# Kernel optimization log

Hardware: AMD Instinct MI355X
Metric: run time of the kernel (lower is better)

## Reference

```python
import jax, jax.numpy as jnp
import numpy as np

DIM = 16
FDIM = 16
KNN = 10
N = 1_000_000


def setup_inputs() -> dict:
    key = jax.random.key(0)
    k1, k2, k3, k4, k5, k6 = jax.random.split(key, 6)
    xknn = jax.random.normal(k1, (N, DIM, KNN), dtype=jnp.float32)
    x = jax.random.normal(k2, (N, DIM), dtype=jnp.float32)
    # mlpF = Conv1d(dim, F, 1): weight [F, dim] (kernel size 1 squeezed), bias [F]
    s = 1.0 / np.sqrt(DIM)
    Wf = jax.random.normal(k3, (FDIM, DIM), dtype=jnp.float32) * s
    bf = jax.random.normal(k4, (FDIM,), dtype=jnp.float32) * s
    # mlp1 = Conv1d(F, 1, 1): weight [F], bias scalar
    s1 = 1.0 / np.sqrt(FDIM)
    W1 = jax.random.normal(k5, (FDIM,), dtype=jnp.float32) * s1
    b1 = jax.random.normal(k6, (), dtype=jnp.float32) * s1
    return {"xknn": xknn, "x": x, "Wf": Wf, "bf": bf, "W1": W1, "b1": b1}


def reference(xknn, x, Wf, bf, W1, b1):
    n = xknn.shape[0]
    x2 = xknn.reshape(n, DIM, KNN)                       # [N, dim, K]
    # mlpF on neighbors: Conv1d(dim->F, k=1)
    h2 = jnp.einsum('fd,ndk->nfk', Wf, x2) + bf[:, None]  # [N, F, K]
    a2 = jnp.einsum('f,nfk->nk', W1, h2)[:, None, :] + b1  # mlp1 -> [N, 1, K]
    # mlpF + mlp1 on center point
    x1 = x.reshape(n, DIM, 1)
    h1 = jnp.einsum('fd,ndk->nfk', Wf, x1) + bf[:, None]   # [N, F, 1]
    a1 = jnp.einsum('f,nfk->nk', W1, h1) + b1              # [N, 1] (squeeze+unsqueeze)
    # per-slice additive attention logits (the python loop in the original)
    logits = a2 + a1[:, :, None]                           # [N, 1, K]
    # torch Fn.softmax with implicit dim on 3D tensor -> dim=0 (faithful)
    xc = jax.nn.softmax(logits, axis=0)                    # [N, 1, K]
    # values: mlpF(x2) again, then a raw reshape [N,F,K]->[N,K,F] (not transpose)
    x2v = h2.reshape(n, KNN, FDIM)                         # [N, K, F]
    x_attn = jnp.matmul(xc, x2v)                           # [N, 1, F]
    return x_attn.squeeze(), x2v
```

## Files before the change

### kernel.cpp

```cpp
#include <hip/hip_runtime.h>
#include <math.h>


__device__ __forceinline__ void comb(float& m, float& s, float om, float os) {
  float M = fmaxf(m, om);
  if (M == -INFINITY) return;
  s = s * __expf(m - M) + os * __expf(om - M);
  m = M;
}

__global__ __launch_bounds__(256) void gap_k1(
    const float* __restrict__ xknn, const float* __restrict__ x,
    const float* __restrict__ Wf, const float* __restrict__ bf,
    const float* __restrict__ W1, const float* __restrict__ b1p,
    float* __restrict__ out, float* __restrict__ partials, int n) {
  __shared__ float s_x2[16][196];
  __shared__ float s_x[16][16];
  __shared__ float s_wf[256];
  __shared__ float s_misc[33];
  __shared__ float s_red[4][10][2];

  const int tid = threadIdx.x;
  const int p = tid >> 4;
  const int f = tid & 15;

  s_wf[tid] = Wf[tid];
  if (tid < 16) s_misc[tid] = bf[tid];
  else if (tid < 32) s_misc[tid] = W1[tid - 16];
  else if (tid == 32) s_misc[32] = b1p[0];
  __syncthreads();

  float wfrow[16];
#pragma unroll
  for (int d = 0; d < 16; ++d) wfrow[d] = s_wf[f * 16 + d];
  const float bff = s_misc[f];
  const float w1f = s_misc[16 + f];
  const float b1v = s_misc[32];

  float run_m = -INFINITY, run_s = 0.f;

  float* out0 = out;
  float* out1 = out + (size_t)n * 16;

  for (int base = blockIdx.x * 16; base < n; base += gridDim.x * 16) {
    __syncthreads();
    const int npts = min(16, n - base);
    const int nf4 = npts * 40;
    for (int idx4 = tid; idx4 < nf4; idx4 += 256) {
      float4 v = *(const float4*)(xknn + (size_t)base * 160 + (size_t)idx4 * 4);
      int pl = idx4 / 40;
      int r0 = (idx4 - pl * 40) * 4;
      float vv[4] = {v.x, v.y, v.z, v.w};
#pragma unroll
      for (int j = 0; j < 4; ++j) {
        int r = r0 + j;
        int d = r / 10;
        int kk = r - d * 10;
        s_x2[pl][d * 12 + kk] = vv[j];
      }
    }
    if (tid < npts * 4) {
      int pl = tid >> 2, c = tid & 3;
      *(float4*)(&s_x[pl][c * 4]) =
          *(const float4*)(x + (size_t)(base + pl) * 16 + (size_t)c * 4);
    }
    __syncthreads();

    float h2f[10];
#pragma unroll
    for (int k = 0; k < 10; ++k) h2f[k] = bff;
#pragma unroll
    for (int d = 0; d < 16; ++d) {
      const float* r = &s_x2[p][d * 12];
      float w = wfrow[d];
      float4 xa = *(const float4*)(r);
      float4 xb = *(const float4*)(r + 4);
      float2 xc2 = *(const float2*)(r + 8);
      h2f[0] = fmaf(w, xa.x, h2f[0]);
      h2f[1] = fmaf(w, xa.y, h2f[1]);
      h2f[2] = fmaf(w, xa.z, h2f[2]);
      h2f[3] = fmaf(w, xa.w, h2f[3]);
      h2f[4] = fmaf(w, xb.x, h2f[4]);
      h2f[5] = fmaf(w, xb.y, h2f[5]);
      h2f[6] = fmaf(w, xb.z, h2f[6]);
      h2f[7] = fmaf(w, xb.w, h2f[7]);
      h2f[8] = fmaf(w, xc2.x, h2f[8]);
      h2f[9] = fmaf(w, xc2.y, h2f[9]);
    }

    float a2[10];
#pragma unroll
    for (int k = 0; k < 10; ++k) a2[k] = w1f * h2f[k];
#pragma unroll
    for (int mask = 1; mask < 16; mask <<= 1) {
#pragma unroll
      for (int k = 0; k < 10; ++k) a2[k] += __shfl_xor(a2[k], mask, 16);
    }

    float h1f = bff;
#pragma unroll
    for (int d = 0; d < 16; ++d) h1f = fmaf(wfrow[d], s_x[p][d], h1f);
    float a1p = w1f * h1f;
#pragma unroll
    for (int mask = 1; mask < 16; mask <<= 1) a1p += __shfl_xor(a1p, mask, 16);

    const float addc = a1p + 2.0f * b1v;

    const int pt = base + p;
    if (pt < n) {
      float* o1 = out1 + (size_t)pt * 160 + f * 10;
      *(float2*)(o1 + 0) = make_float2(h2f[0], h2f[1]);
      *(float2*)(o1 + 2) = make_float2(h2f[2], h2f[3]);
      *(float2*)(o1 + 4) = make_float2(h2f[4], h2f[5]);
      *(float2*)(o1 + 6) = make_float2(h2f[6], h2f[7]);
      *(float2*)(o1 + 8) = make_float2(h2f[8], h2f[9]);
      if (f < 10) {
        float lsel = a2[0];
#pragma unroll
        for (int k = 1; k < 10; ++k) lsel = (f == k) ? a2[k] : lsel;
        lsel += addc;
        out0[(size_t)pt * 16 + f] = lsel;
        comb(run_m, run_s, lsel, 1.0f);
      }
    }
  }

#pragma unroll
  for (int mask = 16; mask < 64; mask <<= 1) {
    float om = __shfl_xor(run_m, mask, 64);
    float os = __shfl_xor(run_s, mask, 64);
    comb(run_m, run_s, om, os);
  }
  const int wave = tid >> 6, lane = tid & 63;
  __syncthreads();
  if (lane < 10) { s_red[wave][lane][0] = run_m; s_red[wave][lane][1] = run_s; }
  __syncthreads();
  if (tid < 10) {
    float m = s_red[0][tid][0], s = s_red[0][tid][1];
    comb(m, s, s_red[1][tid][0], s_red[1][tid][1]);
    comb(m, s, s_red[2][tid][0], s_red[2][tid][1]);
    comb(m, s, s_red[3][tid][0], s_red[3][tid][1]);
    partials[(size_t)blockIdx.x * 20 + tid * 2 + 0] = m;
    partials[(size_t)blockIdx.x * 20 + tid * 2 + 1] = s;
  }
}

__global__ __launch_bounds__(256) void gap_k2(const float* __restrict__ part,
                                              int nb, float* __restrict__ fin) {
  const int k = blockIdx.x;
  const int tid = threadIdx.x;
  float m = -INFINITY, s = 0.f;
  for (int i = tid; i < nb; i += 256)
    comb(m, s, part[(size_t)i * 20 + k * 2], part[(size_t)i * 20 + k * 2 + 1]);
#pragma unroll
  for (int mask = 1; mask < 64; mask <<= 1) {
    float om = __shfl_xor(m, mask, 64);
    float os = __shfl_xor(s, mask, 64);
    comb(m, s, om, os);
  }
  __shared__ float sm[4][2];
  const int wave = tid >> 6, lane = tid & 63;
  if (lane == 0) { sm[wave][0] = m; sm[wave][1] = s; }
  __syncthreads();
  if (tid == 0) {
    for (int w = 1; w < 4; ++w) comb(m, s, sm[w][0], sm[w][1]);
    fin[k * 2 + 0] = m;
    fin[k * 2 + 1] = s;
  }
}

__global__ __launch_bounds__(256) void gap_k3(const float* __restrict__ fin,
                                              float* __restrict__ out, int n) {
  __shared__ float s_fin[20];
  if (threadIdx.x < 20) s_fin[threadIdx.x] = fin[threadIdx.x];
  __syncthreads();
  float mk[10], rsk[10];
#pragma unroll
  for (int k = 0; k < 10; ++k) {
    mk[k] = s_fin[2 * k];
    rsk[k] = 1.0f / s_fin[2 * k + 1];
  }
  float* out0 = out;
  const float* out1 = out + (size_t)n * 16;
  const int q = threadIdx.x & 3;
  const int pl = threadIdx.x >> 2;
  for (long i = (long)blockIdx.x * 64 + pl; i < n; i += (long)gridDim.x * 64) {
    float* lrow = out0 + i * 16;
    float4 la = *(const float4*)(lrow);
    float4 lb = *(const float4*)(lrow + 4);
    float2 lc = *(const float2*)(lrow + 8);
    float l[10] = {la.x, la.y, la.z, la.w, lb.x, lb.y, lb.z, lb.w, lc.x, lc.y};
    float w[10];
#pragma unroll
    for (int k = 0; k < 10; ++k) w[k] = __expf(l[k] - mk[k]) * rsk[k];
    const float* vrow = out1 + i * 160 + q * 4;
    float4 acc = make_float4(0.f, 0.f, 0.f, 0.f);
#pragma unroll
    for (int k = 0; k < 10; ++k) {
      float4 v = *(const float4*)(vrow + k * 16);
      float wk = w[k];
      acc.x = fmaf(wk, v.x, acc.x);
      acc.y = fmaf(wk, v.y, acc.y);
      acc.z = fmaf(wk, v.z, acc.z);
      acc.w = fmaf(wk, v.w, acc.w);
    }
    *(float4*)(lrow + q * 4) = acc;
  }
}

extern "C" void kernel_launch(void* const* d_in, const int* in_sizes, int n_in,
                              void* d_out, int out_size, void* d_ws, size_t ws_size,
                              hipStream_t stream) {
  const float* xknn = (const float*)d_in[0];
  const float* x    = (const float*)d_in[1];
  const float* Wf   = (const float*)d_in[2];
  const float* bf   = (const float*)d_in[3];
  const float* W1   = (const float*)d_in[4];
  const float* b1   = (const float*)d_in[5];
  float* out = (float*)d_out;
  const int n = in_sizes[1] / 16;

  const int G1 = 2048;
  float* partials = (float*)d_ws;
  float* finals = partials + (size_t)G1 * 20;

  gap_k1<<<G1, 256, 0, stream>>>(xknn, x, Wf, bf, W1, b1, out, partials, n);
  gap_k2<<<10, 256, 0, stream>>>(partials, G1, finals);
  gap_k3<<<2048, 256, 0, stream>>>(finals, out, n);
}
```

Baseline: 584.5 us.

## Compute per-point features in registers with quad threads, dropping shared-memory staging

```diff
diff --git a/kernel.cpp b/kernel.cpp
--- a/kernel.cpp
+++ b/kernel.cpp
@@ -14,126 +14,140 @@
     const float* __restrict__ Wf, const float* __restrict__ bf,
     const float* __restrict__ W1, const float* __restrict__ b1p,
     float* __restrict__ out, float* __restrict__ partials, int n) {
-  __shared__ float s_x2[16][196];
-  __shared__ float s_x[16][16];
-  __shared__ float s_wf[256];
-  __shared__ float s_misc[33];
-  __shared__ float s_red[4][10][2];
+  __shared__ float s_red[4][16][2];
 
   const int tid = threadIdx.x;
-  const int p = tid >> 4;
-  const int f = tid & 15;
-
-  s_wf[tid] = Wf[tid];
-  if (tid < 16) s_misc[tid] = bf[tid];
-  else if (tid < 32) s_misc[tid] = W1[tid - 16];
-  else if (tid == 32) s_misc[32] = b1p[0];
-  __syncthreads();
-
-  float wfrow[16];
-#pragma unroll
-  for (int d = 0; d < 16; ++d) wfrow[d] = s_wf[f * 16 + d];
-  const float bff = s_misc[f];
-  const float w1f = s_misc[16 + f];
-  const float b1v = s_misc[32];
-
-  float run_m = -INFINITY, run_s = 0.f;
+  const int q = tid & 3;
+  const int lane = tid & 63;
+  const int wave = tid >> 6;
+
+  float wfq[4][16], w1q[4], bfq[4];
+#pragma unroll
+  for (int fp = 0; fp < 4; ++fp) {
+    const float* wr = Wf + (size_t)(4 * q + fp) * 16;
+#pragma unroll
+    for (int dq = 0; dq < 4; ++dq) {
+      float4 v = *(const float4*)(wr + dq * 4);
+      wfq[fp][dq * 4 + 0] = v.x;
+      wfq[fp][dq * 4 + 1] = v.y;
+      wfq[fp][dq * 4 + 2] = v.z;
+      wfq[fp][dq * 4 + 3] = v.w;
+    }
+    w1q[fp] = W1[4 * q + fp];
+    bfq[fp] = bf[4 * q + fp];
+  }
+  const float b1v = b1p[0];
+
+  float rm[4] = {-INFINITY, -INFINITY, -INFINITY, -INFINITY};
+  float rs[4] = {0.f, 0.f, 0.f, 0.f};
 
   float* out0 = out;
   float* out1 = out + (size_t)n * 16;
 
-  for (int base = blockIdx.x * 16; base < n; base += gridDim.x * 16) {
-    __syncthreads();
-    const int npts = min(16, n - base);
-    const int nf4 = npts * 40;
-    for (int idx4 = tid; idx4 < nf4; idx4 += 256) {
-      float4 v = *(const float4*)(xknn + (size_t)base * 160 + (size_t)idx4 * 4);
-      int pl = idx4 / 40;
-      int r0 = (idx4 - pl * 40) * 4;
-      float vv[4] = {v.x, v.y, v.z, v.w};
-#pragma unroll
-      for (int j = 0; j < 4; ++j) {
-        int r = r0 + j;
-        int d = r / 10;
-        int kk = r - d * 10;
-        s_x2[pl][d * 12 + kk] = vv[j];
+  const long quad0 = (long)blockIdx.x * 64 + (tid >> 2);
+  const long qstride = (long)gridDim.x * 64;
+
+  for (long pt = quad0; pt < n; pt += qstride) {
+    float acc[4][10];
+#pragma unroll
+    for (int fp = 0; fp < 4; ++fp)
+#pragma unroll
+      for (int k = 0; k < 10; ++k) acc[fp][k] = bfq[fp];
+
+    const float* row = xknn + (size_t)pt * 160;
+#pragma unroll
+    for (int w4 = 0; w4 < 40; ++w4) {
+      float4 v = *(const float4*)(row + w4 * 4);
+      float ve[4] = {v.x, v.y, v.z, v.w};
+#pragma unroll
+      for (int e = 0; e < 4; ++e) {
+        const int r = w4 * 4 + e;
+        const int d = r / 10;
+        const int k = r - d * 10;
+#pragma unroll
+        for (int fp = 0; fp < 4; ++fp)
+          acc[fp][k] = fmaf(wfq[fp][d], ve[e], acc[fp][k]);
       }
     }
-    if (tid < npts * 4) {
-      int pl = tid >> 2, c = tid & 3;
-      *(float4*)(&s_x[pl][c * 4]) =
-          *(const float4*)(x + (size_t)(base + pl) * 16 + (size_t)c * 4);
-    }
-    __syncthreads();
-
-    float h2f[10];
-#pragma unroll
-    for (int k = 0; k < 10; ++k) h2f[k] = bff;
-#pragma unroll
-    for (int d = 0; d < 16; ++d) {
-      const float* r = &s_x2[p][d * 12];
-      float w = wfrow[d];
-      float4 xa = *(const float4*)(r);
-      float4 xb = *(const float4*)(r + 4);
-      float2 xc2 = *(const float2*)(r + 8);
-      h2f[0] = fmaf(w, xa.x, h2f[0]);
-      h2f[1] = fmaf(w, xa.y, h2f[1]);
-      h2f[2] = fmaf(w, xa.z, h2f[2]);
-      h2f[3] = fmaf(w, xa.w, h2f[3]);
-      h2f[4] = fmaf(w, xb.x, h2f[4]);
-      h2f[5] = fmaf(w, xb.y, h2f[5]);
-      h2f[6] = fmaf(w, xb.z, h2f[6]);
-      h2f[7] = fmaf(w, xb.w, h2f[7]);
-      h2f[8] = fmaf(w, xc2.x, h2f[8]);
-      h2f[9] = fmaf(w, xc2.y, h2f[9]);
-    }
-
-    float a2[10];
-#pragma unroll
-    for (int k = 0; k < 10; ++k) a2[k] = w1f * h2f[k];
-#pragma unroll
-    for (int mask = 1; mask < 16; mask <<= 1) {
-#pragma unroll
-      for (int k = 0; k < 10; ++k) a2[k] += __shfl_xor(a2[k], mask, 16);
-    }
-
-    float h1f = bff;
-#pragma unroll
-    for (int d = 0; d < 16; ++d) h1f = fmaf(wfrow[d], s_x[p][d], h1f);
-    float a1p = w1f * h1f;
-#pragma unroll
-    for (int mask = 1; mask < 16; mask <<= 1) a1p += __shfl_xor(a1p, mask, 16);
+
+    float pa[10];
+#pragma unroll
+    for (int k = 0; k < 10; ++k) {
+      float t = w1q[0] * acc[0][k];
+      t = fmaf(w1q[1], acc[1][k], t);
+      t = fmaf(w1q[2], acc[2][k], t);
+      t = fmaf(w1q[3], acc[3][k], t);
+      pa[k] = t;
+    }
+#pragma unroll
+    for (int k = 0; k < 10; ++k) pa[k] += __shfl_xor(pa[k], 1);
+#pragma unroll
+    for (int k = 0; k < 10; ++k) pa[k] += __shfl_xor(pa[k], 2);
+
+    const float* xr = x + (size_t)pt * 16;
+    float h1[4];
+#pragma unroll
+    for (int fp = 0; fp < 4; ++fp) h1[fp] = bfq[fp];
+#pragma unroll
+    for (int dq = 0; dq < 4; ++dq) {
+      float4 v = *(const float4*)(xr + dq * 4);
+      float ve[4] = {v.x, v.y, v.z, v.w};
+#pragma unroll
+      for (int e = 0; e < 4; ++e)
+#pragma unroll
+        for (int fp = 0; fp < 4; ++fp)
+          h1[fp] = fmaf(wfq[fp][dq * 4 + e], ve[e], h1[fp]);
+    }
+    float a1p = w1q[0] * h1[0];
+    a1p = fmaf(w1q[1], h1[1], a1p);
+    a1p = fmaf(w1q[2], h1[2], a1p);
+    a1p = fmaf(w1q[3], h1[3], a1p);
+    a1p += __shfl_xor(a1p, 1);
+    a1p += __shfl_xor(a1p, 2);
 
     const float addc = a1p + 2.0f * b1v;
 
-    const int pt = base + p;
-    if (pt < n) {
-      float* o1 = out1 + (size_t)pt * 160 + f * 10;
-      *(float2*)(o1 + 0) = make_float2(h2f[0], h2f[1]);
-      *(float2*)(o1 + 2) = make_float2(h2f[2], h2f[3]);
-      *(float2*)(o1 + 4) = make_float2(h2f[4], h2f[5]);
-      *(float2*)(o1 + 6) = make_float2(h2f[6], h2f[7]);
-      *(float2*)(o1 + 8) = make_float2(h2f[8], h2f[9]);
-      if (f < 10) {
-        float lsel = a2[0];
-#pragma unroll
-        for (int k = 1; k < 10; ++k) lsel = (f == k) ? a2[k] : lsel;
-        lsel += addc;
-        out0[(size_t)pt * 16 + f] = lsel;
-        comb(run_m, run_s, lsel, 1.0f);
-      }
-    }
-  }
-
-#pragma unroll
-  for (int mask = 16; mask < 64; mask <<= 1) {
-    float om = __shfl_xor(run_m, mask, 64);
-    float os = __shfl_xor(run_s, mask, 64);
-    comb(run_m, run_s, om, os);
-  }
-  const int wave = tid >> 6, lane = tid & 63;
-  __syncthreads();
-  if (lane < 10) { s_red[wave][lane][0] = run_m; s_red[wave][lane][1] = run_s; }
+    float lj[4];
+#pragma unroll
+    for (int j = 0; j < 4; ++j) {
+      const int k = 4 * q + j;
+      float v = 0.f;
+#pragma unroll
+      for (int kk = 0; kk < 10; ++kk) v = (kk == k) ? (pa[kk] + addc) : v;
+      lj[j] = v;
+      if (k < 10) comb(rm[j], rs[j], v, 1.0f);
+    }
+    *(float4*)(out0 + (size_t)pt * 16 + 4 * q) =
+        make_float4(lj[0], lj[1], lj[2], lj[3]);
+
+    float vals[40];
+#pragma unroll
+    for (int fp = 0; fp < 4; ++fp)
+#pragma unroll
+      for (int k = 0; k < 10; ++k) vals[fp * 10 + k] = acc[fp][k];
+    float* o1 = out1 + (size_t)pt * 160 + 40 * q;
+#pragma unroll
+    for (int i = 0; i < 10; ++i)
+      *(float4*)(o1 + 4 * i) = make_float4(vals[4 * i + 0], vals[4 * i + 1],
+                                           vals[4 * i + 2], vals[4 * i + 3]);
+  }
+
+#pragma unroll
+  for (int mask = 4; mask < 64; mask <<= 1) {
+#pragma unroll
+    for (int j = 0; j < 4; ++j) {
+      float om = __shfl_xor(rm[j], mask);
+      float os = __shfl_xor(rs[j], mask);
+      comb(rm[j], rs[j], om, os);
+    }
+  }
+  if (lane < 4) {
+#pragma unroll
+    for (int j = 0; j < 4; ++j) {
+      s_red[wave][lane * 4 + j][0] = rm[j];
+      s_red[wave][lane * 4 + j][1] = rs[j];
+    }
+  }
   __syncthreads();
   if (tid < 10) {
     float m = s_red[0][tid][0], s = s_red[0][tid][1];
```

New measurement: 863.5 us. +47.7%, slower.
